# Optimization experiments

Measured on AMD Instinct MI355X. Metric: run time of the kernel, lower is better.

Reference implementation:

```python
import jax, jax.numpy as jnp
import numpy as np

# Quantization constants (match init_kwargs)
A_SCALE = 0.05   # activation scale
W_SCALE = 0.01   # weight scale
A_QN, A_QP = -128, 127  # int8 activation clamp range
STRIDE = (2, 2)
PADDING = ((1, 1), (1, 1))
DILATION = (1, 1)


def setup_inputs() -> dict:
    key = jax.random.key(0)
    kx, kw = jax.random.split(key)
    # Input activations [N, C_in, H, W]
    x = jax.random.normal(kx, (32, 256, 56, 56), dtype=jnp.float32)
    # Int4 weights in [-8, 7], stored as int-valued float32 (unpacked form of weight_packed)
    w = jax.random.randint(kw, (256, 256, 3, 3), -8, 8).astype(jnp.float32)
    return {"x": x, "w": w}


def reference(x, w):
    # Activation int8 quantization: round-half-to-even (matches torch.round), clamp to [a_qn, a_qp]
    x_q = jnp.clip(jnp.round(x / A_SCALE), A_QN, A_QP)
    # Int4xInt8 GEMM over unfolded patches == conv on quantized integer values.
    # Values are small ints so fp32 accumulation is exact (|acc| <= 2304*127*8 < 2^24).
    acc = jax.lax.conv_general_dilated(
        x_q, w,
        window_strides=STRIDE,
        padding=PADDING,
        rhs_dilation=DILATION,
        dimension_numbers=("NCHW", "OIHW", "NCHW"),
    )  # [N, C_out, H_out, W_out] = [32, 256, 28, 28]
    # Dequantize: acc_int32 * (a_scale * w_scale); bias=False; out_dtype=float32
    y = acc * (A_SCALE * W_SCALE)
    return y.astype(jnp.float32)
```

## Files before the change

kernel.cpp:

```cpp
#include <hip/hip_runtime.h>
#include <stdint.h>

typedef int v4i __attribute__((ext_vector_type(4)));

#define N_IMG 32
#define C_IN 256
#define H_IN 56
#define W_IN 56
#define C_OUT 256
#define H_OUT 28
#define W_OUT 28
#define H_PAD 58
#define W_PAD 58
#define SP_TOT (N_IMG*H_OUT*W_OUT)

#define XPAD_BYTES ((size_t)N_IMG*H_PAD*W_PAD*C_IN)


__device__ __forceinline__ void glds16(const int8_t* g, int8_t* l) {
    __builtin_amdgcn_global_load_lds(
        (const __attribute__((address_space(1))) void*)g,
        (__attribute__((address_space(3))) void*)l, 16, 0, 0);
}

__global__ __launch_bounds__(256, 4) void quant_kernel(const float* __restrict__ x,
                                                       int8_t* __restrict__ xpad) {
    __shared__ uint32_t ldsu[W_IN * 65];
    const int hp = blockIdx.x, n = blockIdx.y;
    const int t = threadIdx.x;
    int8_t* row = xpad + ((size_t)n * H_PAD + hp) * W_PAD * C_IN;

    if (hp == 0 || hp == H_PAD - 1) {
        #pragma unroll
        for (int i = 0; i < 4; ++i) {
            int idx = i * 256 + t;
            if (idx < 928) *(int4*)(row + idx * 16) = (int4){0, 0, 0, 0};
        }
        return;
    }
    const int h = hp - 1;
    const float* xrow = x + (size_t)n * (C_IN * H_IN * W_IN) + (size_t)h * W_IN;

    if (t < 32) {
        int8_t* p = (t < 16) ? (row + t * 16)
                             : (row + (size_t)(W_PAD - 1) * C_IN + (t - 16) * 16);
        *(int4*)p = (int4){0, 0, 0, 0};
    }

    const int lane = t & 63, wv = t >> 6;
    const int j = lane >> 4, w4 = lane & 15;
    const int w4c = (w4 < 14) ? w4 : 13;
    #pragma unroll
    for (int i16 = 0; i16 < 16; ++i16) {
        const int c4p = i16 * 4 + wv;
        const float4 v = *(const float4*)(xrow + (size_t)(4 * c4p + j) * (H_IN * W_IN)
                                          + w4c * 4);
        float f[4] = {v.x, v.y, v.z, v.w};
        uint32_t u = 0;
        #pragma unroll
        for (int i = 0; i < 4; ++i) {
            float qv = rintf(f[i] * 20.0f);
            qv = fminf(fmaxf(qv, -128.0f), 127.0f);
            u |= ((uint32_t)((int)qv & 255)) << (8 * i);
        }
        uint32_t p1 = __shfl_xor(u, 16);
        uint32_t tt = (j & 1) ? (((p1 >> 8) & 0x00FF00FFu) | (u & 0xFF00FF00u))
                              : ((u & 0x00FF00FFu) | ((p1 << 8) & 0xFF00FF00u));
        uint32_t p2 = __shfl_xor(tt, 32);
        uint32_t rr = (j & 2) ? ((p2 >> 16) | (tt & 0xFFFF0000u))
                              : ((tt & 0x0000FFFFu) | (p2 << 16));
        if (w4 < 14) ldsu[(w4 * 4 + j) * 65 + c4p] = rr;
    }
    __syncthreads();

    int8_t* op = row + C_IN;
    #pragma unroll
    for (int it = 0; it < 14; ++it) {
        int idx = it * 256 + t;
        int w = idx >> 6, c4 = idx & 63;
        *(uint32_t*)(op + (size_t)w * C_IN + c4 * 4) = ldsu[w * 65 + c4];
    }
}

__global__ __launch_bounds__(256) void wq_kernel(const float* __restrict__ w,
                                                 int8_t* __restrict__ wq) {
    int idx = blockIdx.x * 256 + threadIdx.x;
    int ci  = idx & 255;
    int co  = (idx >> 8) & 255;
    int khw = idx >> 16;
    float v = w[(size_t)(co * C_IN + ci) * 9 + khw];
    wq[idx] = (int8_t)(int)rintf(v);
}

__global__ __launch_bounds__(256) void conv_kernel(const int8_t* __restrict__ xpad,
                                                   const int8_t* __restrict__ wq,
                                                   float* __restrict__ out) {
    __shared__ __align__(16) int8_t lds[32768];
    const int t = threadIdx.x;
    const int wave = t >> 6, lane = t & 63;
    const int q = lane >> 4, s = lane & 15;
    const int co_blk = blockIdx.y * 64;
    const int sp_blk = blockIdx.x * 64;

    const int r0 = t >> 3;
    const int xch = ((t & 7) ^ (r0 & 7)) * 16;
    const int8_t* gw2[2];
    const int8_t* ga2[2];
    #pragma unroll
    for (int jj = 0; jj < 2; ++jj) {
        const int r = r0 + jj * 32;
        gw2[jj] = wq + (size_t)(co_blk + r) * 256 + xch;
        int sp = sp_blk + r;
        int n  = sp / (H_OUT * W_OUT);
        int rm = sp - n * (H_OUT * W_OUT);
        int ho = rm / W_OUT;
        int wo = rm - ho * W_OUT;
        ga2[jj] = xpad + ((size_t)(n * H_PAD + ho * 2) * W_PAD + wo * 2) * C_IN + xch;
    }

    const int cw = (wave >> 1) * 32;
    const int sw = (wave & 1) * 32;
    int out_base[2];
    #pragma unroll
    for (int jj = 0; jj < 2; ++jj) {
        int sp = sp_blk + sw + jj * 16 + s;
        int n  = sp / (H_OUT * W_OUT);
        int rm = sp - n * (H_OUT * W_OUT);
        int ho = rm / W_OUT;
        int wo = rm - ho * W_OUT;
        out_base[jj] = n * (C_OUT * H_OUT * W_OUT) + ho * W_OUT + wo;
    }

    v4i acc[2][2];
    #pragma unroll
    for (int i = 0; i < 2; ++i)
        #pragma unroll
        for (int jj = 0; jj < 2; ++jj)
            acc[i][jj] = (v4i){0, 0, 0, 0};

    auto stage = [&](int hk, int bufb) {
        const int tap = hk >> 1, hf = hk & 1;
        const int wo_ = tap * (C_OUT * C_IN) + hf * 128;
        const int ao_ = ((tap / 3) * W_PAD + (tap % 3)) * C_IN + hf * 128;
        int8_t* lb = lds + bufb * 16384;
        #pragma unroll
        for (int jj = 0; jj < 2; ++jj) {
            glds16(gw2[jj] + wo_, lb + (t + jj * 256) * 16);
            glds16(ga2[jj] + ao_, lb + 8192 + (t + jj * 256) * 16);
        }
    };

    auto compute = [&](int bufb) {
        const int8_t* lb = lds + bufb * 16384;
        #pragma unroll
        for (int ks = 0; ks < 2; ++ks) {
            const int st = ((ks * 4 + q) ^ (s & 7)) * 16;
            v4i a[2], b[2];
            #pragma unroll
            for (int i = 0; i < 2; ++i)
                a[i] = *(const v4i*)(lb + (cw + i * 16 + s) * 128 + st);
            #pragma unroll
            for (int jj = 0; jj < 2; ++jj)
                b[jj] = *(const v4i*)(lb + 8192 + (sw + jj * 16 + s) * 128 + st);
            #pragma unroll
            for (int i = 0; i < 2; ++i)
                #pragma unroll
                for (int jj = 0; jj < 2; ++jj)
                    acc[i][jj] = __builtin_amdgcn_mfma_i32_16x16x64_i8(
                        a[i], b[jj], acc[i][jj], 0, 0, 0);
        }
    };

    stage(0, 0);
    __syncthreads();
    #pragma unroll
    for (int hk = 0; hk < 18; ++hk) {
        const int cb = hk & 1;
        if (hk < 17) stage(hk + 1, cb ^ 1);
        compute(cb);
        if (hk < 17) __syncthreads();
    }

    #pragma unroll
    for (int jj = 0; jj < 2; ++jj) {
        #pragma unroll
        for (int i = 0; i < 2; ++i) {
            const int co0 = co_blk + cw + i * 16 + q * 4;
            #pragma unroll
            for (int r = 0; r < 4; ++r) {
                out[(size_t)out_base[jj] + (size_t)(co0 + r) * (H_OUT * W_OUT)] =
                    (float)acc[i][jj][r] * 0.0005f;
            }
        }
    }
}

extern "C" void kernel_launch(void* const* d_in, const int* in_sizes, int n_in,
                              void* d_out, int out_size, void* d_ws, size_t ws_size,
                              hipStream_t stream) {
    const float* x = (const float*)d_in[0];
    const float* w = (const float*)d_in[1];
    float* out = (float*)d_out;
    int8_t* xpad = (int8_t*)d_ws;
    int8_t* wqb  = xpad + XPAD_BYTES;

    quant_kernel<<<dim3(H_PAD, N_IMG), 256, 0, stream>>>(x, xpad);
    wq_kernel<<<(9 * C_OUT * C_IN) / 256, 256, 0, stream>>>(w, wqb);
    conv_kernel<<<dim3(SP_TOT / 64, C_OUT / 64), 256, 0, stream>>>(xpad, wqb, out);
}
```

Before: 191.2 us.

## Enlarge conv tile to 128 channels with triple-buffered K=64 pipeline and swizzled block order

The conv kernel now computes 128 output channels by 64 spatial positions per block instead of 64x64, so each activation tile is reused across twice as many output channels. The K loop is split into 64-byte slices (36 steps) with a three-slot LDS ring: loads run two stages ahead, and explicit vmcnt waits plus barriers replace the per-step __syncthreads. The 1D grid is remapped so that co-tile pairs and neighbouring spatial tiles land on the same XCD for L2 reuse. The cost is more barriers per unit of work and more accumulator registers per wave, with launch_bounds set to 4 blocks per CU.

```diff
diff --git a/kernel.cpp b/kernel.cpp
--- a/kernel.cpp
+++ b/kernel.cpp
@@ -92,33 +92,33 @@
     wq[idx] = (int8_t)(int)rintf(v);
 }
 
-__global__ __launch_bounds__(256) void conv_kernel(const int8_t* __restrict__ xpad,
-                                                   const int8_t* __restrict__ wq,
-                                                   float* __restrict__ out) {
-    __shared__ __align__(16) int8_t lds[32768];
+__global__ __launch_bounds__(256, 4) void conv_kernel(const int8_t* __restrict__ xpad,
+                                                      const int8_t* __restrict__ wq,
+                                                      float* __restrict__ out) {
+    __shared__ __align__(16) int8_t lds[36864];
     const int t = threadIdx.x;
     const int wave = t >> 6, lane = t & 63;
     const int q = lane >> 4, s = lane & 15;
-    const int co_blk = blockIdx.y * 64;
-    const int sp_blk = blockIdx.x * 64;
-
-    const int r0 = t >> 3;
-    const int xch = ((t & 7) ^ (r0 & 7)) * 16;
-    const int8_t* gw2[2];
-    const int8_t* ga2[2];
-    #pragma unroll
-    for (int jj = 0; jj < 2; ++jj) {
-        const int r = r0 + jj * 32;
-        gw2[jj] = wq + (size_t)(co_blk + r) * 256 + xch;
-        int sp = sp_blk + r;
-        int n  = sp / (H_OUT * W_OUT);
-        int rm = sp - n * (H_OUT * W_OUT);
-        int ho = rm / W_OUT;
-        int wo = rm - ho * W_OUT;
-        ga2[jj] = xpad + ((size_t)(n * H_PAD + ho * 2) * W_PAD + wo * 2) * C_IN + xch;
-    }
-
-    const int cw = (wave >> 1) * 32;
+
+    const int wg = blockIdx.x;
+    const int lg = (wg & 7) * 98 + (wg >> 3);
+    const int co_blk = (lg & 1) * 128;
+    const int sp_blk = (lg >> 1) * 64;
+
+    const int srow = t >> 2;
+    const int scl  = t & 3;
+    const int sq   = scl ^ ((srow >> 1) & 3);
+    const int8_t* gw0 = wq + (size_t)(co_blk + srow) * 256 + sq * 16;
+    const int8_t* gw1 = wq + (size_t)(co_blk + 64 + srow) * 256 + sq * 16;
+    const int spA = sp_blk + srow;
+    const int nA  = spA / (H_OUT * W_OUT);
+    const int rmA = spA - nA * (H_OUT * W_OUT);
+    const int hoA = rmA / W_OUT;
+    const int woA = rmA - hoA * W_OUT;
+    const int8_t* ga = xpad + ((size_t)(nA * H_PAD + hoA * 2) * W_PAD + woA * 2) * C_IN
+                       + sq * 16;
+
+    const int cw = (wave >> 1) * 64;
     const int sw = (wave & 1) * 32;
     int out_base[2];
     #pragma unroll
@@ -131,60 +131,55 @@
         out_base[jj] = n * (C_OUT * H_OUT * W_OUT) + ho * W_OUT + wo;
     }
 
-    v4i acc[2][2];
-    #pragma unroll
-    for (int i = 0; i < 2; ++i)
+    v4i acc[4][2];
+    #pragma unroll
+    for (int i = 0; i < 4; ++i)
         #pragma unroll
         for (int jj = 0; jj < 2; ++jj)
             acc[i][jj] = (v4i){0, 0, 0, 0};
 
-    auto stage = [&](int hk, int bufb) {
-        const int tap = hk >> 1, hf = hk & 1;
-        const int wo_ = tap * (C_OUT * C_IN) + hf * 128;
-        const int ao_ = ((tap / 3) * W_PAD + (tap % 3)) * C_IN + hf * 128;
-        int8_t* lb = lds + bufb * 16384;
-        #pragma unroll
-        for (int jj = 0; jj < 2; ++jj) {
-            glds16(gw2[jj] + wo_, lb + (t + jj * 256) * 16);
-            glds16(ga2[jj] + ao_, lb + 8192 + (t + jj * 256) * 16);
-        }
+    auto stage = [&](int hk, int8_t* lb) {
+        const int tap = hk >> 2, sl = hk & 3;
+        const int wo_ = tap * (C_OUT * C_IN) + sl * 64;
+        const int ao_ = ((tap / 3) * W_PAD + (tap % 3)) * C_IN + sl * 64;
+        glds16(gw0 + wo_, lb + t * 16);
+        glds16(gw1 + wo_, lb + 4096 + t * 16);
+        glds16(ga  + ao_, lb + 8192 + t * 16);
     };
 
-    auto compute = [&](int bufb) {
-        const int8_t* lb = lds + bufb * 16384;
-        #pragma unroll
-        for (int ks = 0; ks < 2; ++ks) {
-            const int st = ((ks * 4 + q) ^ (s & 7)) * 16;
-            v4i a[2], b[2];
-            #pragma unroll
-            for (int i = 0; i < 2; ++i)
-                a[i] = *(const v4i*)(lb + (cw + i * 16 + s) * 128 + st);
+    auto compute = [&](const int8_t* lb) {
+        const int stoff = (q ^ ((s >> 1) & 3)) * 16;
+        v4i a[4], b[2];
+        #pragma unroll
+        for (int i = 0; i < 4; ++i)
+            a[i] = *(const v4i*)(lb + (cw + i * 16 + s) * 64 + stoff);
+        #pragma unroll
+        for (int jj = 0; jj < 2; ++jj)
+            b[jj] = *(const v4i*)(lb + 8192 + (sw + jj * 16 + s) * 64 + stoff);
+        #pragma unroll
+        for (int i = 0; i < 4; ++i)
             #pragma unroll
             for (int jj = 0; jj < 2; ++jj)
-                b[jj] = *(const v4i*)(lb + 8192 + (sw + jj * 16 + s) * 128 + st);
-            #pragma unroll
-            for (int i = 0; i < 2; ++i)
-                #pragma unroll
-                for (int jj = 0; jj < 2; ++jj)
-                    acc[i][jj] = __builtin_amdgcn_mfma_i32_16x16x64_i8(
-                        a[i], b[jj], acc[i][jj], 0, 0, 0);
-        }
+                acc[i][jj] = __builtin_amdgcn_mfma_i32_16x16x64_i8(
+                    a[i], b[jj], acc[i][jj], 0, 0, 0);
     };
 
-    stage(0, 0);
-    __syncthreads();
-    #pragma unroll
-    for (int hk = 0; hk < 18; ++hk) {
-        const int cb = hk & 1;
-        if (hk < 17) stage(hk + 1, cb ^ 1);
-        compute(cb);
-        if (hk < 17) __syncthreads();
+    stage(0, lds);
+    stage(1, lds + 12288);
+    #pragma unroll
+    for (int hk = 0; hk < 36; ++hk) {
+        if (hk < 35)
+            asm volatile("s_waitcnt vmcnt(3)\n\ts_barrier" ::: "memory");
+        else
+            asm volatile("s_waitcnt vmcnt(0)\n\ts_barrier" ::: "memory");
+        if (hk + 2 < 36) stage(hk + 2, lds + ((hk + 2) % 3) * 12288);
+        compute(lds + (hk % 3) * 12288);
     }
 
     #pragma unroll
     for (int jj = 0; jj < 2; ++jj) {
         #pragma unroll
-        for (int i = 0; i < 2; ++i) {
+        for (int i = 0; i < 4; ++i) {
             const int co0 = co_blk + cw + i * 16 + q * 4;
             #pragma unroll
             for (int r = 0; r < 4; ++r) {
@@ -206,5 +201,5 @@
 
     quant_kernel<<<dim3(H_PAD, N_IMG), 256, 0, stream>>>(x, xpad);
     wq_kernel<<<(9 * C_OUT * C_IN) / 256, 256, 0, stream>>>(w, wqb);
-    conv_kernel<<<dim3(SP_TOT / 64, C_OUT / 64), 256, 0, stream>>>(xpad, wqb, out);
-}
+    conv_kernel<<<dim3(784), 256, 0, stream>>>(xpad, wqb, out);
+}
```

Measured after the change: 196.7 us. +2.8%, slower.
